# Kernel tuning notes

Hardware: AMD Instinct MI355X
Metric: run time of the kernel (lower is better)

Reference implementation:

```python
import jax, jax.numpy as jnp
import numpy as np

B, H, T, N = 8, 12, 1024, 256  # N = mlp_internal_dim_multiplier * n_embd // n_head = 4*768//12
THETA = 2.0 ** 16


def _rope(phases, v):
    # interleaved rotate-half: pairs (even, odd) -> (-odd, even), as in torch stack+view
    v_rot = jnp.stack((-v[..., 1::2], v[..., ::2]), axis=-1).reshape(v.shape)
    ang = (phases % 1.0) * (2.0 * jnp.pi)
    return v * jnp.cos(ang) + v_rot * jnp.sin(ang)


def setup_inputs() -> dict:
    key = jax.random.key(0)
    k1, k2 = jax.random.split(key)
    Q = jax.random.normal(k1, (B, H, T, N), dtype=jnp.float32)
    V = jax.random.normal(k2, (B, H, T, N), dtype=jnp.float32)
    # frozen RoPE frequency buffer: pairs share a frequency, theta=2**16 (cycles/position)
    idx = (jnp.arange(N) // 2 * 2).astype(jnp.float32)
    freqs = (THETA ** (-idx / N)).reshape(1, 1, 1, N)
    return {"Q": Q, "V": V, "freqs": freqs}


def reference(Q, V, freqs):
    t = Q.shape[2]
    pos = jnp.arange(t, dtype=freqs.dtype).reshape(1, 1, -1, 1)
    phases = pos * freqs                      # [1,1,T,N]
    QR = _rope(phases, Q)                     # K is Q in Vision-BDH, so KR = QR
    scale = 1.0 / jnp.sqrt(jnp.asarray(Q.shape[-1], Q.dtype))
    scores = jnp.einsum("bhtn,bhsn->bhts", QR, QR) * scale  # [B,H,T,T]
    attn = jax.nn.softmax(scores, axis=-1)
    return jnp.einsum("bhts,bhsn->bhtn", attn, V)
```

## Files before the change

### kernel.cpp

```cpp
#include <hip/hip_runtime.h>
#include <stdint.h>

typedef __attribute__((ext_vector_type(8))) short short8;
typedef __attribute__((ext_vector_type(4))) float f32x4;

#define BH 96
#define T 1024
#define D 256

static __device__ __forceinline__ unsigned short f2bf(float x){
  uint32_t u = __float_as_uint(x);
  uint32_t r = (u + 0x7FFFu + ((u >> 16) & 1u)) >> 16;
  return (unsigned short)r;
}

static __device__ __forceinline__ uint32_t cvtpk_bf16(float lo, float hi){
  uint32_t r;
  asm("v_cvt_pk_bf16_f32 %0, %1, %2" : "=v"(r) : "v"(lo), "v"(hi));
  return r;
}

static __device__ __forceinline__ float exp2_fast(float x){
  float r;
  asm("v_exp_f32 %0, %1" : "=v"(r) : "v"(x));
  return r;
}

static __device__ __forceinline__ void gload_lds16(const void* g, void* l){
  __builtin_amdgcn_global_load_lds((const __attribute__((address_space(1))) void*)g,
                                   (__attribute__((address_space(3))) void*)l, 16, 0, 0);
}

__global__ void k_rope(const float* __restrict__ Q, const float* __restrict__ freqs,
                       unsigned short* __restrict__ QR){
  const float SC = 0.25f * 1.20112241f;
  long idx = (long)blockIdx.x * 256 + threadIdx.x;
  long e = idx * 4;
  int n = (int)(e & (D - 1));
  int t = (int)((e >> 8) & (T - 1));
  float4 q = *(const float4*)(Q + e);
  float f0 = freqs[n];
  float f2 = freqs[n + 2];
  float ph0 = (float)t * f0; ph0 -= floorf(ph0);
  float ph2 = (float)t * f2; ph2 -= floorf(ph2);
  float c0 = __builtin_amdgcn_cosf(ph0), s0 = __builtin_amdgcn_sinf(ph0);
  float c2 = __builtin_amdgcn_cosf(ph2), s2 = __builtin_amdgcn_sinf(ph2);
  float o0 = (q.x * c0 - q.y * s0) * SC;
  float o1 = (q.y * c0 + q.x * s0) * SC;
  float o2 = (q.z * c2 - q.w * s2) * SC;
  float o3 = (q.w * c2 + q.z * s2) * SC;
  ushort4 o;
  o.x = f2bf(o0); o.y = f2bf(o1); o.z = f2bf(o2); o.w = f2bf(o3);
  *(ushort4*)(QR + e) = o;
}

__global__ void k_transpose(const float* __restrict__ V, unsigned short* __restrict__ Vt){
  __shared__ unsigned short L[64 * 66];
  int bid = blockIdx.x;
  int head = bid >> 6;
  int rem = bid & 63;
  int t0 = (rem & 15) * 64;
  int n0 = (rem >> 4) * 64;
  int tid = threadIdx.x;
  const float* Vh = V + (long)head * T * D;
  unsigned short* Vth = Vt + (long)head * T * D;
  int lr = tid >> 4;
  int lc = (tid & 15) * 4;
#pragma unroll
  for (int i = 0; i < 4; ++i){
    int tl = i * 16 + lr;
    float4 v = *(const float4*)(Vh + (long)(t0 + tl) * D + n0 + lc);
    uint32_t w0 = (uint32_t)f2bf(v.x) | ((uint32_t)f2bf(v.y) << 16);
    uint32_t w1 = (uint32_t)f2bf(v.z) | ((uint32_t)f2bf(v.w) << 16);
    *(uint32_t*)&L[tl * 66 + lc]     = w0;
    *(uint32_t*)&L[tl * 66 + lc + 2] = w1;
  }
  __syncthreads();
  int nr = tid >> 3;
  int t8 = (tid & 7) * 8;
#pragma unroll
  for (int i = 0; i < 2; ++i){
    int n_row = i * 32 + nr;
    unsigned short u[8];
#pragma unroll
    for (int j = 0; j < 8; ++j) u[j] = L[(t8 + j) * 66 + n_row];
    uint4 o;
    o.x = (uint32_t)u[0] | ((uint32_t)u[1] << 16);
    o.y = (uint32_t)u[2] | ((uint32_t)u[3] << 16);
    o.z = (uint32_t)u[4] | ((uint32_t)u[5] << 16);
    o.w = (uint32_t)u[6] | ((uint32_t)u[7] << 16);
    *(uint4*)(Vth + (long)(n0 + n_row) * T + t0 + t8) = o;
  }
}

static __device__ __forceinline__ short8 packP(f32x4 st0, f32x4 st1, float m, float& lsum,
                                               int q15, int g){
  float p00 = exp2_fast(st0.x - m), p01 = exp2_fast(st0.y - m);
  float p02 = exp2_fast(st0.z - m), p03 = exp2_fast(st0.w - m);
  float p10 = exp2_fast(st1.x - m), p11 = exp2_fast(st1.y - m);
  float p12 = exp2_fast(st1.z - m), p13 = exp2_fast(st1.w - m);
  lsum += ((p00 + p01) + (p02 + p03)) + ((p10 + p11) + (p12 + p13));
  uint32_t t0w0 = cvtpk_bf16(p00, p01), t0w1 = cvtpk_bf16(p02, p03);
  uint32_t t1w0 = cvtpk_bf16(p10, p11), t1w1 = cvtpk_bf16(p12, p13);
  int s0l = ((g & 1) << 5) | q15;
  int s1l = s0l + 16;
  uint32_t x0 = __shfl(t0w0, s0l), x1 = __shfl(t0w1, s0l);
  uint32_t X0 = __shfl(t1w0, s0l), X1 = __shfl(t1w1, s0l);
  uint32_t y0 = __shfl(t0w0, s1l), y1 = __shfl(t0w1, s1l);
  uint32_t Y0 = __shfl(t1w0, s1l), Y1 = __shfl(t1w1, s1l);
  bool lo = (g < 2);
  uint4 aws;
  aws.x = lo ? x0 : X0;
  aws.y = lo ? x1 : X1;
  aws.z = lo ? y0 : Y0;
  aws.w = lo ? y1 : Y1;
  return __builtin_bit_cast(short8, aws);
}

static __device__ __forceinline__ void softmax2(
    f32x4 s0a, f32x4 s1a, f32x4 s0b, f32x4 s1b,
    float& mA, float& mB, float& lA, float& lB,
    f32x4* accA, f32x4* accB, short8& paA, short8& paB, int q15, int g){
  float lmA = fmaxf(fmaxf(fmaxf(s0a.x, s0a.y), fmaxf(s0a.z, s0a.w)),
                    fmaxf(fmaxf(s1a.x, s1a.y), fmaxf(s1a.z, s1a.w)));
  float lmB = fmaxf(fmaxf(fmaxf(s0b.x, s0b.y), fmaxf(s0b.z, s0b.w)),
                    fmaxf(fmaxf(s1b.x, s1b.y), fmaxf(s1b.z, s1b.w)));
  if (__any((lmA > mA + 11.0f) || (lmB > mB + 11.0f))){
    float tmA = fmaxf(lmA, __shfl_xor(lmA, 16)); tmA = fmaxf(tmA, __shfl_xor(tmA, 32));
    float tmB = fmaxf(lmB, __shfl_xor(lmB, 16)); tmB = fmaxf(tmB, __shfl_xor(tmB, 32));
    float mnA = fmaxf(mA, tmA), mnB = fmaxf(mB, tmB);
    float aA = exp2_fast(mA - mnA), aB = exp2_fast(mB - mnB);
    mA = mnA; mB = mnB;
    lA *= aA; lB *= aB;
#pragma unroll
    for (int nc = 0; nc < 16; ++nc){ accA[nc] *= aA; accB[nc] *= aB; }
  }
  paA = packP(s0a, s1a, mA, lA, q15, g);
  paB = packP(s0b, s1b, mB, lB, q15, g);
}

__global__ __launch_bounds__(256, 2) void k_flash(const unsigned short* __restrict__ QR,
                                                  const unsigned short* __restrict__ Vt,
                                                  float* __restrict__ Out){
  __shared__ short lds[2][16384];
  int tid = threadIdx.x;
  int wid = tid >> 6, lane = tid & 63;
  int q15 = lane & 15, g = lane >> 4;

  int b = blockIdx.x;
  int x = b & 7, s = b >> 3;
  int qt = s & 7, hg = s >> 3;
  int head = hg * 8 + x;

  const unsigned short* qr = QR + (long)head * T * D;
  const unsigned short* vt = Vt + (long)head * T * D;
  int qb = qt * 128 + wid * 32;

  int bK[4], bV[4];
#pragma unroll
  for (int j = 0; j < 4; ++j){
    int i = tid + j * 256;
    bK[j] = (((i >> 9) * 16 + (i & 15)) * 256) + ((i >> 6) & 7) * 32 + ((i >> 4) & 3) * 8;
    bV[j] = ((i >> 6) * 16 + (i & 15)) * 1024 + ((i >> 4) & 3) * 8;
  }

  short8 qfA[8], qfB[8];
#pragma unroll
  for (int c = 0; c < 8; ++c){
    qfA[c] = *(const short8*)(qr + (long)(qb + q15) * D + c * 32 + g * 8);
    qfB[c] = *(const short8*)(qr + (long)(qb + 16 + q15) * D + c * 32 + g * 8);
  }

  f32x4 accA[16], accB[16];
#pragma unroll
  for (int i = 0; i < 16; ++i){
    accA[i] = f32x4{0.f, 0.f, 0.f, 0.f};
    accB[i] = f32x4{0.f, 0.f, 0.f, 0.f};
  }
  float mA = -3e38f, mB = -3e38f, lA = 0.f, lB = 0.f;
  short8 paA, paB;

#pragma unroll
  for (int j = 0; j < 4; ++j){
    int i = tid + j * 256;
    gload_lds16(qr + bK[j], &lds[0][i * 8]);
    gload_lds16(vt + bV[j], &lds[0][8192 + i * 8]);
  }
  asm volatile("s_waitcnt vmcnt(0)" ::: "memory");
  __syncthreads();

  int buf = 0;
  for (int kb = 0; kb < T; kb += 32){
    if (kb + 32 < T){
      const unsigned short* sk = qr + (long)(kb + 32) * 256;
      const unsigned short* sv = vt + (kb + 32);
#pragma unroll
      for (int j = 0; j < 4; ++j){
        int i = tid + j * 256;
        gload_lds16(sk + bK[j], &lds[buf ^ 1][i * 8]);
        gload_lds16(sv + bV[j], &lds[buf ^ 1][8192 + i * 8]);
      }
    }
    const short* ldsK = &lds[buf][0];
    const short* ldsV = &lds[buf][8192];

    f32x4 s0a = f32x4{0.f,0.f,0.f,0.f}, s0b = f32x4{0.f,0.f,0.f,0.f};
    f32x4 s1a = f32x4{0.f,0.f,0.f,0.f}, s1b = f32x4{0.f,0.f,0.f,0.f};
    __builtin_amdgcn_s_setprio(1);
#pragma unroll
    for (int c = 0; c < 8; ++c){
      short8 kf0 = *(const short8*)&ldsK[c * 512 + lane * 8];
      short8 kf1 = *(const short8*)&ldsK[4096 + c * 512 + lane * 8];
      s0a = __builtin_amdgcn_mfma_f32_16x16x32_bf16(kf0, qfA[c], s0a, 0, 0, 0);
      s0b = __builtin_amdgcn_mfma_f32_16x16x32_bf16(kf0, qfB[c], s0b, 0, 0, 0);
      s1a = __builtin_amdgcn_mfma_f32_16x16x32_bf16(kf1, qfA[c], s1a, 0, 0, 0);
      s1b = __builtin_amdgcn_mfma_f32_16x16x32_bf16(kf1, qfB[c], s1b, 0, 0, 0);
    }
    __builtin_amdgcn_s_setprio(0);
    softmax2(s0a, s1a, s0b, s1b, mA, mB, lA, lB, accA, accB, paA, paB, q15, g);
    __builtin_amdgcn_s_setprio(1);
#pragma unroll
    for (int nc = 0; nc < 16; ++nc){
      short8 vf = *(const short8*)&ldsV[nc * 512 + lane * 8];
      accA[nc] = __builtin_amdgcn_mfma_f32_16x16x32_bf16(vf, paA, accA[nc], 0, 0, 0);
      accB[nc] = __builtin_amdgcn_mfma_f32_16x16x32_bf16(vf, paB, accB[nc], 0, 0, 0);
    }
    __builtin_amdgcn_s_setprio(0);
    asm volatile("s_waitcnt vmcnt(0)" ::: "memory");
    __syncthreads();
    buf ^= 1;
  }

  lA += __shfl_xor(lA, 16); lA += __shfl_xor(lA, 32);
  lB += __shfl_xor(lB, 16); lB += __shfl_xor(lB, 32);
  float rA = 1.0f / lA, rB = 1.0f / lB;
  float* opA = Out + (long)head * T * D + (long)(qb + q15) * D + g * 4;
  float* opB = opA + 16 * D;
#pragma unroll
  for (int nc = 0; nc < 16; ++nc){
    f32x4 oa = accA[nc] * rA;
    f32x4 ob = accB[nc] * rB;
    *(f32x4*)(opA + nc * 16) = oa;
    *(f32x4*)(opB + nc * 16) = ob;
  }
}

extern "C" void kernel_launch(void* const* d_in, const int* in_sizes, int n_in,
                              void* d_out, int out_size, void* d_ws, size_t ws_size,
                              hipStream_t stream){
  (void)in_sizes; (void)n_in; (void)out_size; (void)ws_size;
  const float* Q     = (const float*)d_in[0];
  const float* V     = (const float*)d_in[1];
  const float* freqs = (const float*)d_in[2];
  float* Out = (float*)d_out;
  unsigned short* QR = (unsigned short*)d_ws;
  unsigned short* Vt = QR + (size_t)BH * T * D;
  k_rope<<<dim3((BH * T * D) / 4 / 256), dim3(256), 0, stream>>>(Q, freqs, QR);
  k_transpose<<<dim3(BH * 64), dim3(256), 0, stream>>>(V, Vt);
  k_flash<<<dim3(BH * 8), dim3(256), 0, stream>>>(QR, Vt, Out);
}
```

Before: 190.5 us.

## Switch flash attention MFMAs from 16x16x32 to 32x32x16 bf16 tiles

Rewrites the attention inner loop to use 32x32x16 bf16 MFMA instructions instead of 16x16x32. Each wave now owns a single 32-row query tile, and the LDS K/V tile layouts and address offsets are rebuilt to match the new operand fragment shapes. The P-matrix repacking drops from eight cross-lane shuffles per tile to xor-32 swaps, and the row max reduction needs only one shuffle. Larger MFMA tiles cut instruction count and LDS fragment reads per FLOP, but the new layouts may cause LDS bank conflicts and the split QK accumulation (sA+sB) adds extra VGPR pressure.

```diff
diff --git a/kernel.cpp b/kernel.cpp
--- a/kernel.cpp
+++ b/kernel.cpp
@@ -3,6 +3,7 @@
 
 typedef __attribute__((ext_vector_type(8))) short short8;
 typedef __attribute__((ext_vector_type(4))) float f32x4;
+typedef __attribute__((ext_vector_type(16))) float f32x16;
 
 #define BH 96
 #define T 1024
@@ -93,64 +94,18 @@
   }
 }
 
-static __device__ __forceinline__ short8 packP(f32x4 st0, f32x4 st1, float m, float& lsum,
-                                               int q15, int g){
-  float p00 = exp2_fast(st0.x - m), p01 = exp2_fast(st0.y - m);
-  float p02 = exp2_fast(st0.z - m), p03 = exp2_fast(st0.w - m);
-  float p10 = exp2_fast(st1.x - m), p11 = exp2_fast(st1.y - m);
-  float p12 = exp2_fast(st1.z - m), p13 = exp2_fast(st1.w - m);
-  lsum += ((p00 + p01) + (p02 + p03)) + ((p10 + p11) + (p12 + p13));
-  uint32_t t0w0 = cvtpk_bf16(p00, p01), t0w1 = cvtpk_bf16(p02, p03);
-  uint32_t t1w0 = cvtpk_bf16(p10, p11), t1w1 = cvtpk_bf16(p12, p13);
-  int s0l = ((g & 1) << 5) | q15;
-  int s1l = s0l + 16;
-  uint32_t x0 = __shfl(t0w0, s0l), x1 = __shfl(t0w1, s0l);
-  uint32_t X0 = __shfl(t1w0, s0l), X1 = __shfl(t1w1, s0l);
-  uint32_t y0 = __shfl(t0w0, s1l), y1 = __shfl(t0w1, s1l);
-  uint32_t Y0 = __shfl(t1w0, s1l), Y1 = __shfl(t1w1, s1l);
-  bool lo = (g < 2);
-  uint4 aws;
-  aws.x = lo ? x0 : X0;
-  aws.y = lo ? x1 : X1;
-  aws.z = lo ? y0 : Y0;
-  aws.w = lo ? y1 : Y1;
-  return __builtin_bit_cast(short8, aws);
-}
-
-static __device__ __forceinline__ void softmax2(
-    f32x4 s0a, f32x4 s1a, f32x4 s0b, f32x4 s1b,
-    float& mA, float& mB, float& lA, float& lB,
-    f32x4* accA, f32x4* accB, short8& paA, short8& paB, int q15, int g){
-  float lmA = fmaxf(fmaxf(fmaxf(s0a.x, s0a.y), fmaxf(s0a.z, s0a.w)),
-                    fmaxf(fmaxf(s1a.x, s1a.y), fmaxf(s1a.z, s1a.w)));
-  float lmB = fmaxf(fmaxf(fmaxf(s0b.x, s0b.y), fmaxf(s0b.z, s0b.w)),
-                    fmaxf(fmaxf(s1b.x, s1b.y), fmaxf(s1b.z, s1b.w)));
-  if (__any((lmA > mA + 11.0f) || (lmB > mB + 11.0f))){
-    float tmA = fmaxf(lmA, __shfl_xor(lmA, 16)); tmA = fmaxf(tmA, __shfl_xor(tmA, 32));
-    float tmB = fmaxf(lmB, __shfl_xor(lmB, 16)); tmB = fmaxf(tmB, __shfl_xor(tmB, 32));
-    float mnA = fmaxf(mA, tmA), mnB = fmaxf(mB, tmB);
-    float aA = exp2_fast(mA - mnA), aB = exp2_fast(mB - mnB);
-    mA = mnA; mB = mnB;
-    lA *= aA; lB *= aB;
-#pragma unroll
-    for (int nc = 0; nc < 16; ++nc){ accA[nc] *= aA; accB[nc] *= aB; }
-  }
-  paA = packP(s0a, s1a, mA, lA, q15, g);
-  paB = packP(s0b, s1b, mB, lB, q15, g);
-}
-
 __global__ __launch_bounds__(256, 2) void k_flash(const unsigned short* __restrict__ QR,
                                                   const unsigned short* __restrict__ Vt,
                                                   float* __restrict__ Out){
   __shared__ short lds[2][16384];
   int tid = threadIdx.x;
   int wid = tid >> 6, lane = tid & 63;
-  int q15 = lane & 15, g = lane >> 4;
+  int q31 = lane & 31, h = lane >> 5;
 
   int b = blockIdx.x;
-  int x = b & 7, s = b >> 3;
-  int qt = s & 7, hg = s >> 3;
-  int head = hg * 8 + x;
+  int xx = b & 7, sw = b >> 3;
+  int qt = sw & 7, hg = sw >> 3;
+  int head = hg * 8 + xx;
 
   const unsigned short* qr = QR + (long)head * T * D;
   const unsigned short* vt = Vt + (long)head * T * D;
@@ -160,25 +115,21 @@
 #pragma unroll
   for (int j = 0; j < 4; ++j){
     int i = tid + j * 256;
-    bK[j] = (((i >> 9) * 16 + (i & 15)) * 256) + ((i >> 6) & 7) * 32 + ((i >> 4) & 3) * 8;
-    bV[j] = ((i >> 6) * 16 + (i & 15)) * 1024 + ((i >> 4) & 3) * 8;
-  }
-
-  short8 qfA[8], qfB[8];
-#pragma unroll
-  for (int c = 0; c < 8; ++c){
-    qfA[c] = *(const short8*)(qr + (long)(qb + q15) * D + c * 32 + g * 8);
-    qfB[c] = *(const short8*)(qr + (long)(qb + 16 + q15) * D + c * 32 + g * 8);
-  }
-
-  f32x4 accA[16], accB[16];
-#pragma unroll
-  for (int i = 0; i < 16; ++i){
-    accA[i] = f32x4{0.f, 0.f, 0.f, 0.f};
-    accB[i] = f32x4{0.f, 0.f, 0.f, 0.f};
-  }
-  float mA = -3e38f, mB = -3e38f, lA = 0.f, lB = 0.f;
-  short8 paA, paB;
+    int c = i >> 6, s = i & 63;
+    bK[j] = (s & 31) * 256 + (s >> 5) * 8 + c * 16;
+    bV[j] = ((c >> 1) * 32 + (s & 31)) * 1024 + (c & 1) * 16 + (s >> 5) * 8;
+  }
+
+  short8 qf[16];
+#pragma unroll
+  for (int c = 0; c < 16; ++c)
+    qf[c] = *(const short8*)(qr + (long)(qb + q31) * D + c * 16 + h * 8);
+
+  const f32x16 Zv = {0.f,0.f,0.f,0.f,0.f,0.f,0.f,0.f,0.f,0.f,0.f,0.f,0.f,0.f,0.f,0.f};
+  f32x16 acc[8];
+#pragma unroll
+  for (int i = 0; i < 8; ++i) acc[i] = Zv;
+  float m = -3e38f, lsum = 0.f;
 
 #pragma unroll
   for (int j = 0; j < 4; ++j){
@@ -204,44 +155,94 @@
     const short* ldsK = &lds[buf][0];
     const short* ldsV = &lds[buf][8192];
 
-    f32x4 s0a = f32x4{0.f,0.f,0.f,0.f}, s0b = f32x4{0.f,0.f,0.f,0.f};
-    f32x4 s1a = f32x4{0.f,0.f,0.f,0.f}, s1b = f32x4{0.f,0.f,0.f,0.f};
+    f32x16 sA = Zv, sB = Zv;
     __builtin_amdgcn_s_setprio(1);
 #pragma unroll
     for (int c = 0; c < 8; ++c){
-      short8 kf0 = *(const short8*)&ldsK[c * 512 + lane * 8];
-      short8 kf1 = *(const short8*)&ldsK[4096 + c * 512 + lane * 8];
-      s0a = __builtin_amdgcn_mfma_f32_16x16x32_bf16(kf0, qfA[c], s0a, 0, 0, 0);
-      s0b = __builtin_amdgcn_mfma_f32_16x16x32_bf16(kf0, qfB[c], s0b, 0, 0, 0);
-      s1a = __builtin_amdgcn_mfma_f32_16x16x32_bf16(kf1, qfA[c], s1a, 0, 0, 0);
-      s1b = __builtin_amdgcn_mfma_f32_16x16x32_bf16(kf1, qfB[c], s1b, 0, 0, 0);
+      short8 kf = *(const short8*)&ldsK[c * 512 + lane * 8];
+      sA = __builtin_amdgcn_mfma_f32_32x32x16_bf16(kf, qf[c], sA, 0, 0, 0);
+    }
+#pragma unroll
+    for (int c = 8; c < 16; ++c){
+      short8 kf = *(const short8*)&ldsK[c * 512 + lane * 8];
+      sB = __builtin_amdgcn_mfma_f32_32x32x16_bf16(kf, qf[c], sB, 0, 0, 0);
     }
     __builtin_amdgcn_s_setprio(0);
-    softmax2(s0a, s1a, s0b, s1b, mA, mB, lA, lB, accA, accB, paA, paB, q15, g);
+    f32x16 sc = sA + sB;
+
+    float lm = fmaxf(fmaxf(fmaxf(sc[0], sc[1]), fmaxf(sc[2], sc[3])),
+                     fmaxf(fmaxf(sc[4], sc[5]), fmaxf(sc[6], sc[7])));
+    lm = fmaxf(lm, fmaxf(fmaxf(fmaxf(sc[8], sc[9]), fmaxf(sc[10], sc[11])),
+                         fmaxf(fmaxf(sc[12], sc[13]), fmaxf(sc[14], sc[15]))));
+    lm = fmaxf(lm, __shfl_xor(lm, 32));
+    if (__any(lm > m + 11.0f)){
+      float mn = fmaxf(m, lm);
+      float a = exp2_fast(m - mn);
+      m = mn;
+      lsum *= a;
+#pragma unroll
+      for (int nb = 0; nb < 8; ++nb) acc[nb] *= a;
+    }
+    f32x16 p;
+#pragma unroll
+    for (int e = 0; e < 16; ++e) p[e] = exp2_fast(sc[e] - m);
+    lsum += (((p[0]+p[1])+(p[2]+p[3])) + ((p[4]+p[5])+(p[6]+p[7])))
+          + (((p[8]+p[9])+(p[10]+p[11])) + ((p[12]+p[13])+(p[14]+p[15])));
+
+    uint32_t X0 = cvtpk_bf16(p[0],  p[1]);
+    uint32_t X1 = cvtpk_bf16(p[2],  p[3]);
+    uint32_t Y0 = cvtpk_bf16(p[4],  p[5]);
+    uint32_t Y1 = cvtpk_bf16(p[6],  p[7]);
+    uint32_t sX0 = __shfl_xor(X0, 32), sX1 = __shfl_xor(X1, 32);
+    uint32_t sY0 = __shfl_xor(Y0, 32), sY1 = __shfl_xor(Y1, 32);
+    uint4 f0;
+    f0.x = h ? sY0 : X0;
+    f0.y = h ? sY1 : X1;
+    f0.z = h ? Y0  : sX0;
+    f0.w = h ? Y1  : sX1;
+    uint32_t Z0 = cvtpk_bf16(p[8],  p[9]);
+    uint32_t Z1 = cvtpk_bf16(p[10], p[11]);
+    uint32_t W0 = cvtpk_bf16(p[12], p[13]);
+    uint32_t W1 = cvtpk_bf16(p[14], p[15]);
+    uint32_t sZ0 = __shfl_xor(Z0, 32), sZ1 = __shfl_xor(Z1, 32);
+    uint32_t sW0 = __shfl_xor(W0, 32), sW1 = __shfl_xor(W1, 32);
+    uint4 f1;
+    f1.x = h ? sW0 : Z0;
+    f1.y = h ? sW1 : Z1;
+    f1.z = h ? W0  : sZ0;
+    f1.w = h ? W1  : sZ1;
+    short8 pF0 = __builtin_bit_cast(short8, f0);
+    short8 pF1 = __builtin_bit_cast(short8, f1);
+
     __builtin_amdgcn_s_setprio(1);
 #pragma unroll
-    for (int nc = 0; nc < 16; ++nc){
-      short8 vf = *(const short8*)&ldsV[nc * 512 + lane * 8];
-      accA[nc] = __builtin_amdgcn_mfma_f32_16x16x32_bf16(vf, paA, accA[nc], 0, 0, 0);
-      accB[nc] = __builtin_amdgcn_mfma_f32_16x16x32_bf16(vf, paB, accB[nc], 0, 0, 0);
+    for (int nb = 0; nb < 8; ++nb){
+      short8 v0 = *(const short8*)&ldsV[(nb * 2 + 0) * 512 + lane * 8];
+      short8 v1 = *(const short8*)&ldsV[(nb * 2 + 1) * 512 + lane * 8];
+      acc[nb] = __builtin_amdgcn_mfma_f32_32x32x16_bf16(v0, pF0, acc[nb], 0, 0, 0);
+      acc[nb] = __builtin_amdgcn_mfma_f32_32x32x16_bf16(v1, pF1, acc[nb], 0, 0, 0);
     }
     __builtin_amdgcn_s_setprio(0);
+
     asm volatile("s_waitcnt vmcnt(0)" ::: "memory");
     __syncthreads();
     buf ^= 1;
   }
 
-  lA += __shfl_xor(lA, 16); lA += __shfl_xor(lA, 32);
-  lB += __shfl_xor(lB, 16); lB += __shfl_xor(lB, 32);
-  float rA = 1.0f / lA, rB = 1.0f / lB;
-  float* opA = Out + (long)head * T * D + (long)(qb + q15) * D + g * 4;
-  float* opB = opA + 16 * D;
-#pragma unroll
-  for (int nc = 0; nc < 16; ++nc){
-    f32x4 oa = accA[nc] * rA;
-    f32x4 ob = accB[nc] * rB;
-    *(f32x4*)(opA + nc * 16) = oa;
-    *(f32x4*)(opB + nc * 16) = ob;
+  lsum += __shfl_xor(lsum, 32);
+  float r = 1.0f / lsum;
+  float* op = Out + (long)head * T * D + (long)(qb + q31) * D + h * 4;
+#pragma unroll
+  for (int nb = 0; nb < 8; ++nb){
+#pragma unroll
+    for (int rq = 0; rq < 4; ++rq){
+      f32x4 o;
+      o.x = acc[nb][rq * 4 + 0] * r;
+      o.y = acc[nb][rq * 4 + 1] * r;
+      o.z = acc[nb][rq * 4 + 2] * r;
+      o.w = acc[nb][rq * 4 + 3] * r;
+      *(f32x4*)(op + nb * 32 + rq * 8) = o;
+    }
   }
 }
 
```

Measured after the change: 218.2 us. 14.6% more time.

## Use fp16 16x16x16 MFMA for PV to drop P-fragment lane shuffles

Applied to the files above, without the earlier changes.

Converts V to fp16 instead of bf16 and performs the P·V product with two 16x16x16 f16 MFMAs per output chunk, so the exponentiated scores can be fed straight from the QK accumulator layout without the cross-lane shuffles that repacked P. The V tile is staged in LDS with a new layout and read with per-lane half4 loads at a computed offset. This removes 16 shuffles and several selects per iteration, but doubles the number of PV MFMA instructions and uses narrower LDS reads. It also changes the precision of V and P to fp16 with round-toward-zero packing.

```diff
diff --git a/kernel.cpp b/kernel.cpp
--- a/kernel.cpp
+++ b/kernel.cpp
@@ -3,6 +3,7 @@
 
 typedef __attribute__((ext_vector_type(8))) short short8;
 typedef __attribute__((ext_vector_type(4))) float f32x4;
+typedef __attribute__((ext_vector_type(4))) _Float16 half4;
 
 #define BH 96
 #define T 1024
@@ -14,16 +15,26 @@
   return (unsigned short)r;
 }
 
-static __device__ __forceinline__ uint32_t cvtpk_bf16(float lo, float hi){
-  uint32_t r;
-  asm("v_cvt_pk_bf16_f32 %0, %1, %2" : "=v"(r) : "v"(lo), "v"(hi));
-  return r;
+static __device__ __forceinline__ unsigned short f2h(float x){
+  _Float16 h = (_Float16)x;
+  return __builtin_bit_cast(unsigned short, h);
 }
 
 static __device__ __forceinline__ float exp2_fast(float x){
   float r;
   asm("v_exp_f32 %0, %1" : "=v"(r) : "v"(x));
   return r;
+}
+
+static __device__ __forceinline__ uint32_t pkrtz(float a, float b){
+  return __builtin_bit_cast(uint32_t, __builtin_amdgcn_cvt_pkrtz(a, b));
+}
+
+static __device__ __forceinline__ half4 mkhalf4(float a, float b, float c, float d){
+  uint32_t lo = pkrtz(a, b);
+  uint32_t hi = pkrtz(c, d);
+  uint2 u; u.x = lo; u.y = hi;
+  return __builtin_bit_cast(half4, u);
 }
 
 static __device__ __forceinline__ void gload_lds16(const void* g, void* l){
@@ -70,8 +81,8 @@
   for (int i = 0; i < 4; ++i){
     int tl = i * 16 + lr;
     float4 v = *(const float4*)(Vh + (long)(t0 + tl) * D + n0 + lc);
-    uint32_t w0 = (uint32_t)f2bf(v.x) | ((uint32_t)f2bf(v.y) << 16);
-    uint32_t w1 = (uint32_t)f2bf(v.z) | ((uint32_t)f2bf(v.w) << 16);
+    uint32_t w0 = (uint32_t)f2h(v.x) | ((uint32_t)f2h(v.y) << 16);
+    uint32_t w1 = (uint32_t)f2h(v.z) | ((uint32_t)f2h(v.w) << 16);
     *(uint32_t*)&L[tl * 66 + lc]     = w0;
     *(uint32_t*)&L[tl * 66 + lc + 2] = w1;
   }
@@ -83,7 +94,7 @@
     int n_row = i * 32 + nr;
     unsigned short u[8];
 #pragma unroll
-    for (int j = 0; j < 8; ++j) u[j] = L[(t8 + j) * 66 + n_row];
+    for (int jj = 0; jj < 8; ++jj) u[jj] = L[(t8 + jj) * 66 + n_row];
     uint4 o;
     o.x = (uint32_t)u[0] | ((uint32_t)u[1] << 16);
     o.y = (uint32_t)u[2] | ((uint32_t)u[3] << 16);
@@ -91,52 +102,6 @@
     o.w = (uint32_t)u[6] | ((uint32_t)u[7] << 16);
     *(uint4*)(Vth + (long)(n0 + n_row) * T + t0 + t8) = o;
   }
-}
-
-static __device__ __forceinline__ short8 packP(f32x4 st0, f32x4 st1, float m, float& lsum,
-                                               int q15, int g){
-  float p00 = exp2_fast(st0.x - m), p01 = exp2_fast(st0.y - m);
-  float p02 = exp2_fast(st0.z - m), p03 = exp2_fast(st0.w - m);
-  float p10 = exp2_fast(st1.x - m), p11 = exp2_fast(st1.y - m);
-  float p12 = exp2_fast(st1.z - m), p13 = exp2_fast(st1.w - m);
-  lsum += ((p00 + p01) + (p02 + p03)) + ((p10 + p11) + (p12 + p13));
-  uint32_t t0w0 = cvtpk_bf16(p00, p01), t0w1 = cvtpk_bf16(p02, p03);
-  uint32_t t1w0 = cvtpk_bf16(p10, p11), t1w1 = cvtpk_bf16(p12, p13);
-  int s0l = ((g & 1) << 5) | q15;
-  int s1l = s0l + 16;
-  uint32_t x0 = __shfl(t0w0, s0l), x1 = __shfl(t0w1, s0l);
-  uint32_t X0 = __shfl(t1w0, s0l), X1 = __shfl(t1w1, s0l);
-  uint32_t y0 = __shfl(t0w0, s1l), y1 = __shfl(t0w1, s1l);
-  uint32_t Y0 = __shfl(t1w0, s1l), Y1 = __shfl(t1w1, s1l);
-  bool lo = (g < 2);
-  uint4 aws;
-  aws.x = lo ? x0 : X0;
-  aws.y = lo ? x1 : X1;
-  aws.z = lo ? y0 : Y0;
-  aws.w = lo ? y1 : Y1;
-  return __builtin_bit_cast(short8, aws);
-}
-
-static __device__ __forceinline__ void softmax2(
-    f32x4 s0a, f32x4 s1a, f32x4 s0b, f32x4 s1b,
-    float& mA, float& mB, float& lA, float& lB,
-    f32x4* accA, f32x4* accB, short8& paA, short8& paB, int q15, int g){
-  float lmA = fmaxf(fmaxf(fmaxf(s0a.x, s0a.y), fmaxf(s0a.z, s0a.w)),
-                    fmaxf(fmaxf(s1a.x, s1a.y), fmaxf(s1a.z, s1a.w)));
-  float lmB = fmaxf(fmaxf(fmaxf(s0b.x, s0b.y), fmaxf(s0b.z, s0b.w)),
-                    fmaxf(fmaxf(s1b.x, s1b.y), fmaxf(s1b.z, s1b.w)));
-  if (__any((lmA > mA + 11.0f) || (lmB > mB + 11.0f))){
-    float tmA = fmaxf(lmA, __shfl_xor(lmA, 16)); tmA = fmaxf(tmA, __shfl_xor(tmA, 32));
-    float tmB = fmaxf(lmB, __shfl_xor(lmB, 16)); tmB = fmaxf(tmB, __shfl_xor(tmB, 32));
-    float mnA = fmaxf(mA, tmA), mnB = fmaxf(mB, tmB);
-    float aA = exp2_fast(mA - mnA), aB = exp2_fast(mB - mnB);
-    mA = mnA; mB = mnB;
-    lA *= aA; lB *= aB;
-#pragma unroll
-    for (int nc = 0; nc < 16; ++nc){ accA[nc] *= aA; accB[nc] *= aB; }
-  }
-  paA = packP(s0a, s1a, mA, lA, q15, g);
-  paB = packP(s0b, s1b, mB, lB, q15, g);
 }
 
 __global__ __launch_bounds__(256, 2) void k_flash(const unsigned short* __restrict__ QR,
@@ -161,7 +126,7 @@
   for (int j = 0; j < 4; ++j){
     int i = tid + j * 256;
     bK[j] = (((i >> 9) * 16 + (i & 15)) * 256) + ((i >> 6) & 7) * 32 + ((i >> 4) & 3) * 8;
-    bV[j] = ((i >> 6) * 16 + (i & 15)) * 1024 + ((i >> 4) & 3) * 8;
+    bV[j] = (i & 255) * 1024 + (i >> 8) * 8;
   }
 
   short8 qfA[8], qfB[8];
@@ -178,7 +143,8 @@
     accB[i] = f32x4{0.f, 0.f, 0.f, 0.f};
   }
   float mA = -3e38f, mB = -3e38f, lA = 0.f, lB = 0.f;
-  short8 paA, paB;
+
+  int vbase = (g >> 1) * 2048 + q15 * 8 + (g & 1) * 4;
 
 #pragma unroll
   for (int j = 0; j < 4; ++j){
@@ -202,7 +168,7 @@
       }
     }
     const short* ldsK = &lds[buf][0];
-    const short* ldsV = &lds[buf][8192];
+    const _Float16* ldsVh = (const _Float16*)&lds[buf][8192];
 
     f32x4 s0a = f32x4{0.f,0.f,0.f,0.f}, s0b = f32x4{0.f,0.f,0.f,0.f};
     f32x4 s1a = f32x4{0.f,0.f,0.f,0.f}, s1b = f32x4{0.f,0.f,0.f,0.f};
@@ -217,15 +183,48 @@
       s1b = __builtin_amdgcn_mfma_f32_16x16x32_bf16(kf1, qfB[c], s1b, 0, 0, 0);
     }
     __builtin_amdgcn_s_setprio(0);
-    softmax2(s0a, s1a, s0b, s1b, mA, mB, lA, lB, accA, accB, paA, paB, q15, g);
+
+    float lmA = fmaxf(fmaxf(fmaxf(s0a.x, s0a.y), fmaxf(s0a.z, s0a.w)),
+                      fmaxf(fmaxf(s1a.x, s1a.y), fmaxf(s1a.z, s1a.w)));
+    float lmB = fmaxf(fmaxf(fmaxf(s0b.x, s0b.y), fmaxf(s0b.z, s0b.w)),
+                      fmaxf(fmaxf(s1b.x, s1b.y), fmaxf(s1b.z, s1b.w)));
+    if (__any((lmA > mA + 11.0f) || (lmB > mB + 11.0f))){
+      float tmA = fmaxf(lmA, __shfl_xor(lmA, 16)); tmA = fmaxf(tmA, __shfl_xor(tmA, 32));
+      float tmB = fmaxf(lmB, __shfl_xor(lmB, 16)); tmB = fmaxf(tmB, __shfl_xor(tmB, 32));
+      float mnA = fmaxf(mA, tmA), mnB = fmaxf(mB, tmB);
+      float aA = exp2_fast(mA - mnA), aB = exp2_fast(mB - mnB);
+      mA = mnA; mB = mnB;
+      lA *= aA; lB *= aB;
+#pragma unroll
+      for (int nc = 0; nc < 16; ++nc){ accA[nc] *= aA; accB[nc] *= aB; }
+    }
+    float pa0 = exp2_fast(s0a.x - mA), pa1 = exp2_fast(s0a.y - mA);
+    float pa2 = exp2_fast(s0a.z - mA), pa3 = exp2_fast(s0a.w - mA);
+    float pa4 = exp2_fast(s1a.x - mA), pa5 = exp2_fast(s1a.y - mA);
+    float pa6 = exp2_fast(s1a.z - mA), pa7 = exp2_fast(s1a.w - mA);
+    float pb0 = exp2_fast(s0b.x - mB), pb1 = exp2_fast(s0b.y - mB);
+    float pb2 = exp2_fast(s0b.z - mB), pb3 = exp2_fast(s0b.w - mB);
+    float pb4 = exp2_fast(s1b.x - mB), pb5 = exp2_fast(s1b.y - mB);
+    float pb6 = exp2_fast(s1b.z - mB), pb7 = exp2_fast(s1b.w - mB);
+    lA += ((pa0 + pa1) + (pa2 + pa3)) + ((pa4 + pa5) + (pa6 + pa7));
+    lB += ((pb0 + pb1) + (pb2 + pb3)) + ((pb4 + pb5) + (pb6 + pb7));
+    half4 pA0 = mkhalf4(pa0, pa1, pa2, pa3);
+    half4 pA1 = mkhalf4(pa4, pa5, pa6, pa7);
+    half4 pB0 = mkhalf4(pb0, pb1, pb2, pb3);
+    half4 pB1 = mkhalf4(pb4, pb5, pb6, pb7);
+
     __builtin_amdgcn_s_setprio(1);
 #pragma unroll
     for (int nc = 0; nc < 16; ++nc){
-      short8 vf = *(const short8*)&ldsV[nc * 512 + lane * 8];
-      accA[nc] = __builtin_amdgcn_mfma_f32_16x16x32_bf16(vf, paA, accA[nc], 0, 0, 0);
-      accB[nc] = __builtin_amdgcn_mfma_f32_16x16x32_bf16(vf, paB, accB[nc], 0, 0, 0);
+      half4 v0 = *(const half4*)&ldsVh[vbase + nc * 128];
+      half4 v1 = *(const half4*)&ldsVh[vbase + 4096 + nc * 128];
+      accA[nc] = __builtin_amdgcn_mfma_f32_16x16x16f16(v0, pA0, accA[nc], 0, 0, 0);
+      accA[nc] = __builtin_amdgcn_mfma_f32_16x16x16f16(v1, pA1, accA[nc], 0, 0, 0);
+      accB[nc] = __builtin_amdgcn_mfma_f32_16x16x16f16(v0, pB0, accB[nc], 0, 0, 0);
+      accB[nc] = __builtin_amdgcn_mfma_f32_16x16x16f16(v1, pB1, accB[nc], 0, 0, 0);
     }
     __builtin_amdgcn_s_setprio(0);
+
     asm volatile("s_waitcnt vmcnt(0)" ::: "memory");
     __syncthreads();
     buf ^= 1;
```

Result: slower. 214.1 us (+12.4%).

## Load V fragments directly from global memory instead of staging through LDS

Applied to the files above, without the earlier changes.

V tiles are no longer copied into shared memory. Each lane instead reads its bf16 V fragments straight from the transposed V in global memory, in four groups interleaved with the PV MFMAs. This halves LDS use per block, which may allow higher occupancy, and removes the LDS round trip for V. In exchange every wave in a block re-reads the same V data from global memory or cache, and global load latency now sits in the compute loop, partly hidden by prefetching the first group before the softmax.

```diff
diff --git a/kernel.cpp b/kernel.cpp
--- a/kernel.cpp
+++ b/kernel.cpp
@@ -83,7 +83,7 @@
     int n_row = i * 32 + nr;
     unsigned short u[8];
 #pragma unroll
-    for (int j = 0; j < 8; ++j) u[j] = L[(t8 + j) * 66 + n_row];
+    for (int jj = 0; jj < 8; ++jj) u[jj] = L[(t8 + jj) * 66 + n_row];
     uint4 o;
     o.x = (uint32_t)u[0] | ((uint32_t)u[1] << 16);
     o.y = (uint32_t)u[2] | ((uint32_t)u[3] << 16);
@@ -142,7 +142,7 @@
 __global__ __launch_bounds__(256, 2) void k_flash(const unsigned short* __restrict__ QR,
                                                   const unsigned short* __restrict__ Vt,
                                                   float* __restrict__ Out){
-  __shared__ short lds[2][16384];
+  __shared__ short lds[2][8192];
   int tid = threadIdx.x;
   int wid = tid >> 6, lane = tid & 63;
   int q15 = lane & 15, g = lane >> 4;
@@ -156,13 +156,14 @@
   const unsigned short* vt = Vt + (long)head * T * D;
   int qb = qt * 128 + wid * 32;
 
-  int bK[4], bV[4];
+  int bK[4];
 #pragma unroll
   for (int j = 0; j < 4; ++j){
     int i = tid + j * 256;
     bK[j] = (((i >> 9) * 16 + (i & 15)) * 256) + ((i >> 6) & 7) * 32 + ((i >> 4) & 3) * 8;
-    bV[j] = ((i >> 6) * 16 + (i & 15)) * 1024 + ((i >> 4) & 3) * 8;
-  }
+  }
+
+  const unsigned short* vrow = vt + (long)q15 * T + g * 8;
 
   short8 qfA[8], qfB[8];
 #pragma unroll
@@ -178,13 +179,11 @@
     accB[i] = f32x4{0.f, 0.f, 0.f, 0.f};
   }
   float mA = -3e38f, mB = -3e38f, lA = 0.f, lB = 0.f;
-  short8 paA, paB;
 
 #pragma unroll
   for (int j = 0; j < 4; ++j){
     int i = tid + j * 256;
     gload_lds16(qr + bK[j], &lds[0][i * 8]);
-    gload_lds16(vt + bV[j], &lds[0][8192 + i * 8]);
   }
   asm volatile("s_waitcnt vmcnt(0)" ::: "memory");
   __syncthreads();
@@ -193,16 +192,14 @@
   for (int kb = 0; kb < T; kb += 32){
     if (kb + 32 < T){
       const unsigned short* sk = qr + (long)(kb + 32) * 256;
-      const unsigned short* sv = vt + (kb + 32);
 #pragma unroll
       for (int j = 0; j < 4; ++j){
         int i = tid + j * 256;
         gload_lds16(sk + bK[j], &lds[buf ^ 1][i * 8]);
-        gload_lds16(sv + bV[j], &lds[buf ^ 1][8192 + i * 8]);
       }
     }
     const short* ldsK = &lds[buf][0];
-    const short* ldsV = &lds[buf][8192];
+    const unsigned short* vp = vrow + kb;
 
     f32x4 s0a = f32x4{0.f,0.f,0.f,0.f}, s0b = f32x4{0.f,0.f,0.f,0.f};
     f32x4 s1a = f32x4{0.f,0.f,0.f,0.f}, s1b = f32x4{0.f,0.f,0.f,0.f};
@@ -217,15 +214,50 @@
       s1b = __builtin_amdgcn_mfma_f32_16x16x32_bf16(kf1, qfB[c], s1b, 0, 0, 0);
     }
     __builtin_amdgcn_s_setprio(0);
+
+    short8 vf0[4];
+#pragma unroll
+    for (int r = 0; r < 4; ++r)
+      vf0[r] = *(const short8*)(vp + (long)r * 16 * T);
+
+    short8 paA, paB;
     softmax2(s0a, s1a, s0b, s1b, mA, mB, lA, lB, accA, accB, paA, paB, q15, g);
+
     __builtin_amdgcn_s_setprio(1);
-#pragma unroll
-    for (int nc = 0; nc < 16; ++nc){
-      short8 vf = *(const short8*)&ldsV[nc * 512 + lane * 8];
-      accA[nc] = __builtin_amdgcn_mfma_f32_16x16x32_bf16(vf, paA, accA[nc], 0, 0, 0);
-      accB[nc] = __builtin_amdgcn_mfma_f32_16x16x32_bf16(vf, paB, accB[nc], 0, 0, 0);
+    short8 vf1[4];
+#pragma unroll
+    for (int r = 0; r < 4; ++r)
+      vf1[r] = *(const short8*)(vp + (long)(4 + r) * 16 * T);
+#pragma unroll
+    for (int nc = 0; nc < 4; ++nc){
+      accA[nc] = __builtin_amdgcn_mfma_f32_16x16x32_bf16(vf0[nc], paA, accA[nc], 0, 0, 0);
+      accB[nc] = __builtin_amdgcn_mfma_f32_16x16x32_bf16(vf0[nc], paB, accB[nc], 0, 0, 0);
+    }
+    short8 vf2[4];
+#pragma unroll
+    for (int r = 0; r < 4; ++r)
+      vf2[r] = *(const short8*)(vp + (long)(8 + r) * 16 * T);
+#pragma unroll
+    for (int nc = 0; nc < 4; ++nc){
+      accA[4 + nc] = __builtin_amdgcn_mfma_f32_16x16x32_bf16(vf1[nc], paA, accA[4 + nc], 0, 0, 0);
+      accB[4 + nc] = __builtin_amdgcn_mfma_f32_16x16x32_bf16(vf1[nc], paB, accB[4 + nc], 0, 0, 0);
+    }
+    short8 vf3[4];
+#pragma unroll
+    for (int r = 0; r < 4; ++r)
+      vf3[r] = *(const short8*)(vp + (long)(12 + r) * 16 * T);
+#pragma unroll
+    for (int nc = 0; nc < 4; ++nc){
+      accA[8 + nc] = __builtin_amdgcn_mfma_f32_16x16x32_bf16(vf2[nc], paA, accA[8 + nc], 0, 0, 0);
+      accB[8 + nc] = __builtin_amdgcn_mfma_f32_16x16x32_bf16(vf2[nc], paB, accB[8 + nc], 0, 0, 0);
+    }
+#pragma unroll
+    for (int nc = 0; nc < 4; ++nc){
+      accA[12 + nc] = __builtin_amdgcn_mfma_f32_16x16x32_bf16(vf3[nc], paA, accA[12 + nc], 0, 0, 0);
+      accB[12 + nc] = __builtin_amdgcn_mfma_f32_16x16x32_bf16(vf3[nc], paB, accB[12 + nc], 0, 0, 0);
     }
     __builtin_amdgcn_s_setprio(0);
+
     asm volatile("s_waitcnt vmcnt(0)" ::: "memory");
     __syncthreads();
     buf ^= 1;
```

After: 511.7 us. 169% more time.
